# Kernel tuning notes

Measured on AMD Instinct MI355X. Metric: run time of the kernel, lower is better.

The kernel has to match this reference:

```python
import jax, jax.numpy as jnp
import numpy as np


def setup_inputs() -> dict:
    key = jax.random.key(0)
    x = jax.random.normal(key, (8, 2048, 1024), dtype=jnp.float32)
    return {"x": x}


def reference(x):
    # softmax over the sequence axis (dim=-2)
    visual = jax.nn.softmax(x, axis=-2)  # [B, S, D]
    # 2D FFT: fft over last dim, then over dim -2; keep real part only
    out = jnp.fft.fft(jnp.fft.fft(visual, axis=-1), axis=-2).real
    return (out, visual)
```

## Files before the change

kernel.cpp:

```cpp
#include <hip/hip_runtime.h>
#include <math.h>

#define BB 8
#define SS 2048
#define DD 1024

typedef float nf2 __attribute__((ext_vector_type(2)));

__device__ __forceinline__ float2 ntload2(const float2* p) {
    nf2 v = __builtin_nontemporal_load((const nf2*)p);
    return make_float2(v.x, v.y);
}

__device__ __forceinline__ float2 cmul(float2 a, float2 b) {
    return make_float2(fmaf(a.x, b.x, -a.y * b.y), fmaf(a.x, b.y, a.y * b.x));
}
__device__ __forceinline__ float2 c_add(float2 a, float2 b){ return make_float2(a.x+b.x, a.y+b.y); }
__device__ __forceinline__ float2 c_sub(float2 a, float2 b){ return make_float2(a.x-b.x, a.y-b.y); }
__device__ __forceinline__ float2 c_mi(float2 a){ return make_float2(a.y, -a.x); }

__device__ __forceinline__ void dft4(float2 c0, float2 c1, float2 c2, float2 c3,
                                     float2& o0, float2& o1, float2& o2, float2& o3) {
    float2 d0 = c_add(c0, c2), d1 = c_sub(c0, c2);
    float2 d2 = c_add(c1, c3), d3 = c_mi(c_sub(c1, c3));
    o0 = c_add(d0, d2); o1 = c_add(d1, d3); o2 = c_sub(d0, d2); o3 = c_sub(d1, d3);
}

__device__ __forceinline__ void dft16(float2* z) {
    float2 a[16];
    #pragma unroll
    for (int r0 = 0; r0 < 4; ++r0)
        dft4(z[r0], z[r0+4], z[r0+8], z[r0+12], a[4*r0], a[4*r0+1], a[4*r0+2], a[4*r0+3]);
    const float2 W1 = {0.9238795325f, -0.3826834324f};
    const float2 W2 = {0.7071067812f, -0.7071067812f};
    const float2 W3 = {0.3826834324f, -0.9238795325f};
    const float2 W6 = {-0.7071067812f, -0.7071067812f};
    const float2 W9 = {-0.9238795325f, 0.3826834324f};
    a[5]  = cmul(a[5],  W1); a[6]  = cmul(a[6],  W2); a[7]  = cmul(a[7],  W3);
    a[9]  = cmul(a[9],  W2); a[10] = c_mi(a[10]);     a[11] = cmul(a[11], W6);
    a[13] = cmul(a[13], W3); a[14] = cmul(a[14], W6); a[15] = cmul(a[15], W9);
    #pragma unroll
    for (int m = 0; m < 4; ++m)
        dft4(a[m], a[4+m], a[8+m], a[12+m], z[m], z[m+4], z[m+8], z[m+12]);
}

__device__ __forceinline__ void dft8(const float2* u, float2* X) {
    float2 A0,A1,A2,A3,B0,B1,B2,B3;
    dft4(u[0], u[2], u[4], u[6], A0, A1, A2, A3);
    dft4(u[1], u[3], u[5], u[7], B0, B1, B2, B3);
    const float r = 0.7071067812f;
    float2 W1B = make_float2(r*(B1.x + B1.y), r*(B1.y - B1.x));
    float2 W2B = c_mi(B2);
    float2 W3B = make_float2(r*(B3.y - B3.x), -r*(B3.x + B3.y));
    X[0] = c_add(A0, B0);  X[4] = c_sub(A0, B0);
    X[1] = c_add(A1, W1B); X[5] = c_sub(A1, W1B);
    X[2] = c_add(A2, W2B); X[6] = c_sub(A2, W2B);
    X[3] = c_add(A3, W3B); X[7] = c_sub(A3, W3B);
}

__global__ __launch_bounds__(256) void k_sumexp_partial(const float* __restrict__ x,
                                                        float* __restrict__ partial) {
    int bid = blockIdx.x;
    int b  = bid >> 6;
    int sc = bid & 63;
    const float4* xp = (const float4*)(x + ((size_t)(b * SS + sc * 32)) * DD) + threadIdx.x;
    float4 acc = make_float4(0.f, 0.f, 0.f, 0.f);
    #pragma unroll 8
    for (int i = 0; i < 32; ++i) {
        float4 v = xp[(size_t)i * (DD / 4)];
        acc.x += __expf(v.x); acc.y += __expf(v.y);
        acc.z += __expf(v.z); acc.w += __expf(v.w);
    }
    ((float4*)(partial + (size_t)(b * 64 + sc) * DD))[threadIdx.x] = acc;
}

__global__ __launch_bounds__(256) void k_sumexp_combine(const float* __restrict__ partial,
                                                        float* __restrict__ rsum) {
    int i = blockIdx.x * 256 + threadIdx.x;
    int b = i >> 8, d4 = i & 255;
    const float4* p = (const float4*)(partial + (size_t)b * 64 * DD) + d4;
    float4 s = make_float4(0.f, 0.f, 0.f, 0.f);
    #pragma unroll 8
    for (int sc = 0; sc < 64; ++sc) {
        float4 v = p[(size_t)sc * (DD / 4)];
        s.x += v.x; s.y += v.y; s.z += v.z; s.w += v.w;
    }
    ((float4*)rsum)[i] = make_float4(1.f/s.x, 1.f/s.y, 1.f/s.z, 1.f/s.w);
}

#define RB 1040
__global__ __launch_bounds__(256, 4) void k_fft_d(const float* __restrict__ x,
                                                  const float* __restrict__ rsum,
                                                  float* __restrict__ visual,
                                                  float2* __restrict__ V1) {
    __shared__ float2 buf[4 * RB];
    const int t = threadIdx.x;
    const int row = t >> 6;
    const int tr  = t & 63;
    const int s4  = blockIdx.x << 2;
    const int b   = s4 >> 11;
    const int sl  = (s4 & (SS - 1)) + row;
    const float* rs = rsum + b * DD;
    float2* rbuf = buf + row * RB;

    float2 z[16];
    {
        const int q = tr;
        const float* xr = x + (size_t)(s4 + row) * DD;
        float* vr = visual + (size_t)(s4 + row) * DD;
        #pragma unroll
        for (int r = 0; r < 16; ++r) {
            int d = q + 64 * r;
            float xv = __builtin_nontemporal_load(xr + d);
            float v = __expf(xv) * rs[d];
            __builtin_nontemporal_store(v, vr + d);
            z[r] = make_float2(v, 0.f);
        }
        dft16(z);
        float sn, cs;
        __sincosf(-6.283185307179586f * (float)q / 1024.f, &sn, &cs);
        float2 w = make_float2(cs, sn), wk = w;
        #pragma unroll
        for (int k1 = 1; k1 < 16; ++k1) { z[k1] = cmul(z[k1], wk); wk = cmul(wk, w); }
        #pragma unroll
        for (int k1 = 0; k1 < 16; ++k1) rbuf[65 * k1 + q] = z[k1];
    }
    __syncthreads();
    {
        const int k1 = tr & 15, q1 = tr >> 4;
        const float2* p = rbuf + 65 * k1 + q1;
        #pragma unroll
        for (int j = 0; j < 16; ++j) z[j] = p[4 * j];
        __syncthreads();
        dft16(z);
        float sn, cs;
        __sincosf(-6.283185307179586f * (float)q1 / 64.f, &sn, &cs);
        float2 w = make_float2(cs, sn), wk = w;
        #pragma unroll
        for (int a = 1; a < 16; ++a) { z[a] = cmul(z[a], wk); wk = cmul(wk, w); }
        float2* p2 = rbuf + 65 * k1 + 16 * q1;
        #pragma unroll
        for (int a = 0; a < 16; ++a) p2[a] = z[a];
    }
    __syncthreads();
    {
        const int k1 = tr & 15, j = tr >> 4;
        float2* v1b = V1 + ((size_t)b * 128 * SS + sl) * 4;
        #pragma unroll
        for (int jj = 0; jj < 4; ++jj) {
            const int k2a = 4 * j + jj;
            const float2* p = rbuf + 65 * k1 + k2a;
            float2 X0, X1, X2, X3;
            dft4(p[0], p[16], p[32], p[48], X0, X1, X2, X3);
            const int kb = k1 + 16 * k2a;
            float2 v0 = (kb == 0) ? make_float2(X0.x, X2.x)
                                  : X0;
            v1b[(size_t)(kb >> 2) * (SS * 4) + (kb & 3)] = v0;
            const int kb1 = kb + 256;
            v1b[(size_t)(kb1 >> 2) * (SS * 4) + (kb1 & 3)] = X1;
        }
    }
}

#define CS1 2072
#define CS2 2232
__global__ __launch_bounds__(512, 4) void k_fft_s(const float2* __restrict__ V1,
                                                  float* __restrict__ out,
                                                  float2* __restrict__ Zcol) {
    __shared__ float2 buf[4 * CS2];
    const int t = threadIdx.x;
    const int b = blockIdx.x & 7;
    const int G = blockIdx.x >> 3;

    float2 z[16];
    {
        const int c = t & 3, q = t >> 2;
        const float2* srcp = V1 + (size_t)(b * 128 + G) * (SS * 4);
        #pragma unroll
        for (int r = 0; r < 16; ++r)
            z[r] = ntload2(srcp + t + 512 * r);
        dft16(z);
        float sn, cs;
        __sincosf(-6.283185307179586f * (float)q / 2048.f, &sn, &cs);
        float2 w = make_float2(cs, sn), wk = w;
        #pragma unroll
        for (int k1 = 1; k1 < 16; ++k1) { z[k1] = cmul(z[k1], wk); wk = cmul(wk, w); }
        float2* p = buf + c * CS1 + q;
        #pragma unroll
        for (int k1 = 0; k1 < 16; ++k1) p[129 * k1] = z[k1];
    }
    __syncthreads();

    {
        const int k1 = t & 15, c = (t >> 4) & 3, q1 = t >> 6;
        const float2* p = buf + c * CS1 + 129 * k1 + q1;
        #pragma unroll
        for (int j = 0; j < 16; ++j) z[j] = p[8 * j];
        __syncthreads();
        dft16(z);
        float sn, cs;
        __sincosf(-6.283185307179586f * (float)q1 / 128.f, &sn, &cs);
        float2 w = make_float2(cs, sn), wk = w;
        #pragma unroll
        for (int a = 1; a < 16; ++a) { z[a] = cmul(z[a], wk); wk = cmul(wk, w); }
        float2* p2 = buf + c * CS2 + 280 * q1 + 17 * k1;
        #pragma unroll
        for (int a = 0; a < 16; ++a) p2[a] = z[a];
    }
    __syncthreads();

    const int c = t & 3, rest = t >> 2;
    const int k1 = rest & 15, k2h = rest >> 4;
    const int k2col = 4 * G + c;
    float* outb = out + (size_t)b * SS * DD;
    float2* Zb = Zcol + b * SS;
    const bool packed = (k2col == 0);
    #pragma unroll
    for (int e = 0; e < 2; ++e) {
        const int k2a = 2 * k2h + e;
        float2 u[8], X[8];
        const float2* p = buf + c * CS2 + 17 * k1 + k2a;
        #pragma unroll
        for (int q1 = 0; q1 < 8; ++q1) u[q1] = p[280 * q1];
        dft8(u, X);
        #pragma unroll
        for (int k2b = 0; k2b < 8; ++k2b) {
            const int k = k1 + 16 * k2a + 256 * k2b;
            if (packed) {
                Zb[k] = X[k2b];
            } else {
                outb[(size_t)k * DD + k2col] = X[k2b].x;
                outb[(size_t)((SS - k) & (SS - 1)) * DD + (DD - k2col)] = X[k2b].x;
            }
        }
    }
    if (G == 0) {
        __syncthreads();
        #pragma unroll
        for (int i = 0; i < 4; ++i) {
            const int k  = t + (i << 9);
            const int km = (SS - k) & (SS - 1);
            float2 Zk = Zb[k], Zm = Zb[km];
            outb[(size_t)k * DD]       = 0.5f * (Zk.x + Zm.x);
            outb[(size_t)k * DD + 512] = 0.5f * (Zk.y + Zm.y);
        }
    }
}

extern "C" void kernel_launch(void* const* d_in, const int* in_sizes, int n_in,
                              void* d_out, int out_size, void* d_ws, size_t ws_size,
                              hipStream_t stream) {
    const float* x = (const float*)d_in[0];
    float* out    = (float*)d_out;
    float* visual = out + (size_t)BB * SS * DD;

    char* ws = (char*)d_ws;
    float2* V1   = (float2*)ws;
    float2* Zcol = (float2*)(ws + (size_t)BB * 128 * SS * 4 * sizeof(float2));
    float* partial = (float*)(Zcol + BB * SS);
    float* rsum    = partial + (size_t)BB * 64 * DD;

    hipLaunchKernelGGL(k_sumexp_partial, dim3(BB * 64), dim3(256), 0, stream, x, partial);
    hipLaunchKernelGGL(k_sumexp_combine, dim3(8), dim3(256), 0, stream, partial, rsum);
    hipLaunchKernelGGL(k_fft_d, dim3(BB * SS / 4), dim3(256), 0, stream, x, rsum, visual, V1);
    hipLaunchKernelGGL(k_fft_s, dim3(BB * 128), dim3(512), 0, stream, V1, out, Zcol);
}
```

Baseline: 96.29 us.

## Fuse softmax sum reduction into row-FFT kernel with per-batch atomic barrier

Merges the partial exp-sum, combine, and row-FFT kernels into one persistent-style kernel of 512 blocks. Each block reduces its 32-row chunk, the last block per batch computes the reciprocal sums, and every block spin-waits on a per-batch atomic counter before doing the FFT for its own 32 rows, so that chunk is still in cache. This removes two kernel launches and is meant to let re-reading x hit in cache. The cost is a grid-wide spin wait that assumes all 64 blocks of a batch are resident at once, plus much less parallelism per block (8 iterations over 512 blocks instead of 4096 blocks), and an extra memset launch.

```diff
diff --git a/kernel.cpp b/kernel.cpp
--- a/kernel.cpp
+++ b/kernel.cpp
@@ -58,107 +58,122 @@
     X[3] = c_add(A3, W3B); X[7] = c_sub(A3, W3B);
 }
 
-__global__ __launch_bounds__(256) void k_sumexp_partial(const float* __restrict__ x,
-                                                        float* __restrict__ partial) {
-    int bid = blockIdx.x;
-    int b  = bid >> 6;
-    int sc = bid & 63;
-    const float4* xp = (const float4*)(x + ((size_t)(b * SS + sc * 32)) * DD) + threadIdx.x;
-    float4 acc = make_float4(0.f, 0.f, 0.f, 0.f);
-    #pragma unroll 8
-    for (int i = 0; i < 32; ++i) {
-        float4 v = xp[(size_t)i * (DD / 4)];
-        acc.x += __expf(v.x); acc.y += __expf(v.y);
-        acc.z += __expf(v.z); acc.w += __expf(v.w);
-    }
-    ((float4*)(partial + (size_t)(b * 64 + sc) * DD))[threadIdx.x] = acc;
-}
-
-__global__ __launch_bounds__(256) void k_sumexp_combine(const float* __restrict__ partial,
-                                                        float* __restrict__ rsum) {
-    int i = blockIdx.x * 256 + threadIdx.x;
-    int b = i >> 8, d4 = i & 255;
-    const float4* p = (const float4*)(partial + (size_t)b * 64 * DD) + d4;
-    float4 s = make_float4(0.f, 0.f, 0.f, 0.f);
-    #pragma unroll 8
-    for (int sc = 0; sc < 64; ++sc) {
-        float4 v = p[(size_t)sc * (DD / 4)];
-        s.x += v.x; s.y += v.y; s.z += v.z; s.w += v.w;
-    }
-    ((float4*)rsum)[i] = make_float4(1.f/s.x, 1.f/s.y, 1.f/s.z, 1.f/s.w);
-}
-
 #define RB 1040
-__global__ __launch_bounds__(256, 4) void k_fft_d(const float* __restrict__ x,
-                                                  const float* __restrict__ rsum,
-                                                  float* __restrict__ visual,
-                                                  float2* __restrict__ V1) {
+__global__ __launch_bounds__(256, 2) void k_sm_fft_d(const float* __restrict__ x,
+                                                     float* __restrict__ visual,
+                                                     float2* __restrict__ V1,
+                                                     float* __restrict__ partial,
+                                                     float* __restrict__ rsum,
+                                                     unsigned int* __restrict__ cnt) {
     __shared__ float2 buf[4 * RB];
-    const int t = threadIdx.x;
+    __shared__ unsigned int sdone;
+    const int t   = threadIdx.x;
+    const int bid = blockIdx.x;
+    const int b   = bid >> 6;
+    const int sc  = bid & 63;
+
+    {
+        const float4* xp = (const float4*)(x + ((size_t)(b * SS + sc * 32)) * DD) + t;
+        float4 acc = make_float4(0.f, 0.f, 0.f, 0.f);
+        #pragma unroll 8
+        for (int i = 0; i < 32; ++i) {
+            float4 v = xp[(size_t)i * (DD / 4)];
+            acc.x += __expf(v.x); acc.y += __expf(v.y);
+            acc.z += __expf(v.z); acc.w += __expf(v.w);
+        }
+        ((float4*)(partial + (size_t)(b * 64 + sc) * DD))[t] = acc;
+    }
+    __threadfence();
+    __syncthreads();
+    if (t == 0) sdone = atomicAdd(&cnt[b], 1u);
+    __syncthreads();
+
+    if (sdone == 63u) {
+        __threadfence();
+        const float4* p = (const float4*)(partial + (size_t)b * 64 * DD) + t;
+        float4 s = make_float4(0.f, 0.f, 0.f, 0.f);
+        #pragma unroll 8
+        for (int scc = 0; scc < 64; ++scc) {
+            float4 v = p[(size_t)scc * (DD / 4)];
+            s.x += v.x; s.y += v.y; s.z += v.z; s.w += v.w;
+        }
+        ((float4*)(rsum + b * DD))[t] = make_float4(1.f/s.x, 1.f/s.y, 1.f/s.z, 1.f/s.w);
+        __threadfence();
+        __syncthreads();
+        if (t == 0) atomicAdd(&cnt[b], 1u);
+    }
+    if (t == 0) {
+        while (__hip_atomic_load(&cnt[b], __ATOMIC_ACQUIRE, __HIP_MEMORY_SCOPE_AGENT) < 65u)
+            __builtin_amdgcn_s_sleep(8);
+    }
+    __syncthreads();
+
     const int row = t >> 6;
     const int tr  = t & 63;
-    const int s4  = blockIdx.x << 2;
-    const int b   = s4 >> 11;
-    const int sl  = (s4 & (SS - 1)) + row;
     const float* rs = rsum + b * DD;
     float2* rbuf = buf + row * RB;
-
-    float2 z[16];
-    {
-        const int q = tr;
-        const float* xr = x + (size_t)(s4 + row) * DD;
-        float* vr = visual + (size_t)(s4 + row) * DD;
-        #pragma unroll
-        for (int r = 0; r < 16; ++r) {
-            int d = q + 64 * r;
-            float xv = __builtin_nontemporal_load(xr + d);
-            float v = __expf(xv) * rs[d];
-            __builtin_nontemporal_store(v, vr + d);
-            z[r] = make_float2(v, 0.f);
-        }
-        dft16(z);
-        float sn, cs;
-        __sincosf(-6.283185307179586f * (float)q / 1024.f, &sn, &cs);
-        float2 w = make_float2(cs, sn), wk = w;
-        #pragma unroll
-        for (int k1 = 1; k1 < 16; ++k1) { z[k1] = cmul(z[k1], wk); wk = cmul(wk, w); }
-        #pragma unroll
-        for (int k1 = 0; k1 < 16; ++k1) rbuf[65 * k1 + q] = z[k1];
-    }
-    __syncthreads();
-    {
-        const int k1 = tr & 15, q1 = tr >> 4;
-        const float2* p = rbuf + 65 * k1 + q1;
-        #pragma unroll
-        for (int j = 0; j < 16; ++j) z[j] = p[4 * j];
-        __syncthreads();
-        dft16(z);
-        float sn, cs;
-        __sincosf(-6.283185307179586f * (float)q1 / 64.f, &sn, &cs);
-        float2 w = make_float2(cs, sn), wk = w;
-        #pragma unroll
-        for (int a = 1; a < 16; ++a) { z[a] = cmul(z[a], wk); wk = cmul(wk, w); }
-        float2* p2 = rbuf + 65 * k1 + 16 * q1;
-        #pragma unroll
-        for (int a = 0; a < 16; ++a) p2[a] = z[a];
-    }
-    __syncthreads();
-    {
-        const int k1 = tr & 15, j = tr >> 4;
-        float2* v1b = V1 + ((size_t)b * 128 * SS + sl) * 4;
-        #pragma unroll
-        for (int jj = 0; jj < 4; ++jj) {
-            const int k2a = 4 * j + jj;
-            const float2* p = rbuf + 65 * k1 + k2a;
-            float2 X0, X1, X2, X3;
-            dft4(p[0], p[16], p[32], p[48], X0, X1, X2, X3);
-            const int kb = k1 + 16 * k2a;
-            float2 v0 = (kb == 0) ? make_float2(X0.x, X2.x)
-                                  : X0;
-            v1b[(size_t)(kb >> 2) * (SS * 4) + (kb & 3)] = v0;
-            const int kb1 = kb + 256;
-            v1b[(size_t)(kb1 >> 2) * (SS * 4) + (kb1 & 3)] = X1;
-        }
+    float2* v1b = V1 + (size_t)b * 128 * SS * 4;
+
+    for (int it = 0; it < 8; ++it) {
+        const int sl = sc * 32 + (it << 2) + row;
+        float2 z[16];
+        {
+            const int q = tr;
+            const float* xr = x + ((size_t)b * SS + sl) * DD;
+            float* vr = visual + ((size_t)b * SS + sl) * DD;
+            #pragma unroll
+            for (int r = 0; r < 16; ++r) {
+                int d = q + 64 * r;
+                float xv = __builtin_nontemporal_load(xr + d);
+                float v = __expf(xv) * rs[d];
+                __builtin_nontemporal_store(v, vr + d);
+                z[r] = make_float2(v, 0.f);
+            }
+            dft16(z);
+            float sn, cs;
+            __sincosf(-6.283185307179586f * (float)q / 1024.f, &sn, &cs);
+            float2 w = make_float2(cs, sn), wk = w;
+            #pragma unroll
+            for (int k1 = 1; k1 < 16; ++k1) { z[k1] = cmul(z[k1], wk); wk = cmul(wk, w); }
+            #pragma unroll
+            for (int k1 = 0; k1 < 16; ++k1) rbuf[65 * k1 + q] = z[k1];
+        }
+        __syncthreads();
+        {
+            const int k1 = tr & 15, q1 = tr >> 4;
+            const float2* p = rbuf + 65 * k1 + q1;
+            #pragma unroll
+            for (int j = 0; j < 16; ++j) z[j] = p[4 * j];
+            __syncthreads();
+            dft16(z);
+            float sn, cs;
+            __sincosf(-6.283185307179586f * (float)q1 / 64.f, &sn, &cs);
+            float2 w = make_float2(cs, sn), wk = w;
+            #pragma unroll
+            for (int a = 1; a < 16; ++a) { z[a] = cmul(z[a], wk); wk = cmul(wk, w); }
+            float2* p2 = rbuf + 65 * k1 + 16 * q1;
+            #pragma unroll
+            for (int a = 0; a < 16; ++a) p2[a] = z[a];
+        }
+        __syncthreads();
+        {
+            const int k1 = tr & 15, j = tr >> 4;
+            float2* v1r = v1b + (size_t)sl * 4;
+            #pragma unroll
+            for (int jj = 0; jj < 4; ++jj) {
+                const int k2a = 4 * j + jj;
+                const float2* p = rbuf + 65 * k1 + k2a;
+                float2 X0, X1, X2, X3;
+                dft4(p[0], p[16], p[32], p[48], X0, X1, X2, X3);
+                const int kb = k1 + 16 * k2a;
+                float2 v0 = (kb == 0) ? make_float2(X0.x, X2.x)
+                                      : X0;
+                v1r[(size_t)(kb >> 2) * (SS * 4) + (kb & 3)] = v0;
+                const int kb1 = kb + 256;
+                v1r[(size_t)(kb1 >> 2) * (SS * 4) + (kb1 & 3)] = X1;
+            }
+        }
+        __syncthreads();
     }
 }
 
@@ -259,9 +274,10 @@
     float2* Zcol = (float2*)(ws + (size_t)BB * 128 * SS * 4 * sizeof(float2));
     float* partial = (float*)(Zcol + BB * SS);
     float* rsum    = partial + (size_t)BB * 64 * DD;
-
-    hipLaunchKernelGGL(k_sumexp_partial, dim3(BB * 64), dim3(256), 0, stream, x, partial);
-    hipLaunchKernelGGL(k_sumexp_combine, dim3(8), dim3(256), 0, stream, partial, rsum);
-    hipLaunchKernelGGL(k_fft_d, dim3(BB * SS / 4), dim3(256), 0, stream, x, rsum, visual, V1);
+    unsigned int* cnt = (unsigned int*)(rsum + BB * DD);
+
+    hipMemsetAsync(cnt, 0, BB * sizeof(unsigned int), stream);
+    hipLaunchKernelGGL(k_sm_fft_d, dim3(BB * 64), dim3(256), 0, stream,
+                       x, visual, V1, partial, rsum, cnt);
     hipLaunchKernelGGL(k_fft_s, dim3(BB * 128), dim3(512), 0, stream, V1, out, Zcol);
 }
```

After: 285.4 us. 2.96x slower.
